# Performance work log

Hardware: AMD Instinct MI355X
Metric: run time of the kernel (lower is better)

Reference implementation:

```python
import jax, jax.numpy as jnp
import numpy as np

TEMPERATURE = 12.5
SINK_EPS = 0.05
SINK_ITERS = 100


def setup_inputs() -> dict:
    key = jax.random.key(0)
    k1, k2, k3, k4 = jax.random.split(key, 4)
    b, n_way, k_shot, q, c, h, w = 8, 5, 1, 75, 640, 7, 7
    return {
        "support_xf": jax.random.normal(k1, (b, n_way * k_shot, c, h, w), jnp.float32),
        "query_xf": jax.random.normal(k2, (b, q, c, h, w), jnp.float32),
        "support_y": jax.random.randint(k3, (b, n_way * k_shot), 0, n_way),
        "query_y": jax.random.randint(k4, (b, q), 0, n_way),
        "n_way": n_way,
        "k_shot": k_shot,
    }


def _sinkhorn_flow(cost, log_a, log_b, eps=SINK_EPS, iters=SINK_ITERS):
    """Entropic-OT (Sinkhorn, log-domain) replacement for cv2.EMD.
    cost: [..., m, n]; log_a: [..., m]; log_b: [..., n] (log of prob marginals).
    Returns transport plan P with row sums ~ exp(log_a), col sums ~ exp(log_b)."""
    f = jnp.zeros_like(log_a)
    g = jnp.zeros_like(log_b)

    def body(_, fg):
        f, g = fg
        f = eps * (log_a - jax.nn.logsumexp((g[..., None, :] - cost) / eps, axis=-1))
        g = eps * (log_b - jax.nn.logsumexp((f[..., :, None] - cost) / eps, axis=-2))
        return (f, g)

    f, g = jax.lax.fori_loop(0, iters, body, (f, g))
    return jnp.exp((f[..., :, None] + g[..., None, :] - cost) / eps)


def _deep_emd_logits(support, query):
    # support: [b, p, c, h, w] (1 prototype per class), query: [b, q, c, h, w]
    b, p, c, h, w = support.shape
    q = query.shape[1]
    hw = h * w
    sup = support.reshape(b, p, c, hw)
    qry = query.reshape(b, q, c, hw)

    # get_weight_vector: inner product of local features with the other set's GAP vector
    sup_gap = sup.mean(-1)  # [b, p, c]
    qry_gap = qry.mean(-1)  # [b, q, c]
    w1 = jax.nn.relu(jnp.einsum('bqcm,bpc->bqpm', qry, sup_gap)) + 1e-3  # [b,q,p,hw]
    w2 = jax.nn.relu(jnp.einsum('bpcn,bqc->bqpn', sup, qry_gap)) + 1e-3  # [b,q,p,hw] (weight_2[j,i] transposed)

    # normalize_feature: subtract per-image channel mean; then cosine similarity over channels
    supn = sup - sup.mean(2, keepdims=True)
    qryn = qry - qry.mean(2, keepdims=True)
    supn = supn / jnp.maximum(jnp.linalg.norm(supn, axis=2, keepdims=True), 1e-8)
    qryn = qryn / jnp.maximum(jnp.linalg.norm(qryn, axis=2, keepdims=True), 1e-8)
    S = jnp.einsum('bqcm,bpcn->bqpmn', qryn, supn)  # [b,q,p,hw,hw]

    # emd_inference marginal normalization: relu(w)+1e-5, rescaled so sum = hw -> prob = w/sum(w)
    wa = w1 + 1e-5
    wb = w2 + 1e-5
    log_a = jnp.log(wa) - jnp.log(wa.sum(-1, keepdims=True))
    log_b = jnp.log(wb) - jnp.log(wb.sum(-1, keepdims=True))

    flow = _sinkhorn_flow(1.0 - S, log_a, log_b) * hw  # total mass = hw as in cv2.EMD path
    flow = jax.lax.stop_gradient(flow)  # original flow comes from numpy -> constant

    logits = (S * flow).sum((-2, -1)) * (TEMPERATURE / hw)  # [b, q, p]
    return logits.reshape(b * q, p)


def reference(support_xf, query_xf, support_y, query_y, n_way, k_shot):
    # training / 1-shot path: pick first shot per class
    b = support_xf.shape[0]
    c, h, w = support_xf.shape[2:]
    sup = support_xf.reshape(b, n_way, k_shot, c, h, w)[:, :, 0]
    logits = _deep_emd_logits(sup, query_xf)  # [b*q, n_way]
    labels = query_y.reshape(-1)
    logp = jax.nn.log_softmax(logits, axis=-1)
    loss = -jnp.take_along_axis(logp, labels[:, None], axis=1).mean()
    return loss
```

## Files before the change

kernel.cpp:

```cpp
#include <hip/hip_runtime.h>
#include <math.h>

#define BB 8
#define PP 5
#define QQ 75
#define CC 640
#define HW 49
#define NIMG_Q (BB*QQ)
#define NIMG_S (BB*PP)
#define NPROB  (BB*QQ*PP)
#define TEMP 12.5f

#define CHUNKS 20
#define TROW 16
#define TCH  (HW*TROW)
#define TIMG (CHUNKS*TCH)
#define SROW 25
#define SPROB (HW*SROW)

#define OFF_SGAP   0
#define OFF_QGAP   (OFF_SGAP  + NIMG_S*CC)
#define OFF_SMEAN  (OFF_QGAP  + NIMG_Q*CC)
#define OFF_SINV   (OFF_SMEAN + NIMG_S*HW)
#define OFF_QMEAN  (OFF_SINV  + NIMG_S*HW)
#define OFF_QINV   (OFF_QMEAN + NIMG_Q*HW)
#define OFF_MARGA  (OFF_QINV  + NIMG_Q*HW)
#define OFF_MARGB  (OFF_MARGA + NPROB*HW)
#define OFF_QT     (OFF_MARGB + NPROB*HW)
#define OFF_ST     (OFF_QT    + NIMG_Q*TIMG)
#define OFF_S16    (OFF_ST    + NIMG_S*TIMG)
#define OFF_LOGITS (OFF_S16   + NPROB*SPROB)

typedef _Float16 f16x8 __attribute__((ext_vector_type(8)));
typedef float f32x4 __attribute__((ext_vector_type(4)));
#define MFMAH __builtin_amdgcn_mfma_f32_16x16x32_f16

__device__ __forceinline__ float wsum64(float v) {
#pragma unroll
    for (int off = 32; off > 0; off >>= 1) v += __shfl_xor(v, off, 64);
    return v;
}
__device__ __forceinline__ float rlf(float x, int l) {
    return __int_as_float(__builtin_amdgcn_readlane(__float_as_int(x), l));
}
__device__ __forceinline__ unsigned packh2(float a, float b) {
    union { _Float16 h[2]; unsigned u; } pk;
    pk.h[0] = (_Float16)a; pk.h[1] = (_Float16)b;
    return pk.u;
}
__device__ __forceinline__ float f16lo(unsigned w) {
    union { unsigned short s; _Float16 h; } u; u.s = (unsigned short)w; return (float)u.h;
}
__device__ __forceinline__ float f16hi(unsigned w) {
    union { unsigned short s; _Float16 h; } u; u.s = (unsigned short)(w >> 16); return (float)u.h;
}

__global__ __launch_bounds__(512) __attribute__((amdgpu_waves_per_eu(4, 4)))
void sup_prep(const float* __restrict__ sup, float* __restrict__ ws) {
    int img = blockIdx.x;
    int tid = threadIdx.x;
    int lane = tid & 63;
    int wv = tid >> 6;
    const float* X = sup + (size_t)img * CC * HW;
    float* gap = ws + OFF_SGAP + img * CC;

    __shared__ float cs_p[8][52], sq_p[8][52];
    __shared__ float muL[52], invL[52];
    float cs = 0.f, sq = 0.f;
    if (lane < HW) {
        for (int c8 = wv * 80; c8 < wv * 80 + 80; c8 += 8) {
            float v[8];
#pragma unroll
            for (int j = 0; j < 8; j++) v[j] = X[(c8 + j) * HW + lane];
#pragma unroll
            for (int j = 0; j < 8; j++) {
                cs += v[j];
                sq = fmaf(v[j], v[j], sq);
            }
        }
    }
    if (lane < 52) {
        cs_p[wv][lane] = (lane < HW) ? cs : 0.f;
        sq_p[wv][lane] = (lane < HW) ? sq : 0.f;
    }
    __syncthreads();
    if (wv == 0 && lane < HW) {
        float c4 = 0.f, s4 = 0.f;
#pragma unroll
        for (int w = 0; w < 8; w++) { c4 += cs_p[w][lane]; s4 += sq_p[w][lane]; }
        float mu = c4 * (1.0f / CC);
        float nsq = fmaxf(s4 - c4 * c4 * (1.0f / CC), 0.f);
        float inv = 1.0f / fmaxf(sqrtf(nsq), 1e-8f);
        ws[OFF_SMEAN + img * HW + lane] = mu;
        ws[OFF_SINV + img * HW + lane] = inv;
        muL[lane] = mu;
        invL[lane] = inv;
    }
    for (int c = tid; c < CC; c += 512) {
        const float* row = X + c * HW;
        float s = 0.f;
#pragma unroll
        for (int g = 0; g < 6; g++) {
            float rv[8];
#pragma unroll
            for (int j = 0; j < 8; j++) rv[j] = row[g * 8 + j];
#pragma unroll
            for (int j = 0; j < 8; j++) s += rv[j];
        }
        s += row[48];
        gap[c] = s * (1.0f / HW);
    }
    __syncthreads();
    unsigned* T = (unsigned*)ws + OFF_ST + (size_t)img * TIMG;
    int m = lane;
    if (m < HW) {
        float mu = muL[m], inv = invL[m];
        for (int t = wv; t < CHUNKS; t += 8) {
            float va[32];
#pragma unroll
            for (int j = 0; j < 32; j++) va[j] = X[(t * 32 + j) * HW + m];
            unsigned pk[16];
#pragma unroll
            for (int w = 0; w < 16; w++)
                pk[w] = packh2((va[2 * w] - mu) * inv, (va[2 * w + 1] - mu) * inv);
            uint4* dst = (uint4*)(T + t * TCH + m * TROW);
#pragma unroll
            for (int u = 0; u < 4; u++)
                dst[u] = make_uint4(pk[4 * u], pk[4 * u + 1], pk[4 * u + 2], pk[4 * u + 3]);
        }
    }
}

__global__ __launch_bounds__(512) __attribute__((amdgpu_waves_per_eu(4, 4)))
void qry_prep(const float* __restrict__ qry, float* __restrict__ ws) {
    int img = blockIdx.x;
    int b = img / QQ;
    int tid = threadIdx.x;
    int lane = tid & 63;
    int wv = tid >> 6;
    const float* X = qry + (size_t)img * CC * HW;
    const float* sg = ws + OFF_SGAP + b * PP * CC;
    float* gap = ws + OFF_QGAP + img * CC;

    __shared__ float XSG[PP * CC];
    __shared__ float cs_p[8][52], sq_p[8][52];
    __shared__ float part[8][PP][52];
    __shared__ float muL[52], invL[52];

    for (int i = tid; i < PP * CC / 4; i += 512)
        ((float4*)XSG)[i] = ((const float4*)sg)[i];
    __syncthreads();

    float cs = 0.f, sq = 0.f;
    float acc[PP] = {0.f, 0.f, 0.f, 0.f, 0.f};
    if (lane < HW) {
        for (int c8 = wv * 80; c8 < wv * 80 + 80; c8 += 8) {
            float v[8];
#pragma unroll
            for (int j = 0; j < 8; j++) v[j] = X[(c8 + j) * HW + lane];
#pragma unroll
            for (int j = 0; j < 8; j++) {
                cs += v[j];
                sq = fmaf(v[j], v[j], sq);
            }
#pragma unroll
            for (int p = 0; p < PP; p++) {
                float4 g0 = *(const float4*)&XSG[p * CC + c8];
                float4 g1 = *(const float4*)&XSG[p * CC + c8 + 4];
                float a = acc[p];
                a = fmaf(v[0], g0.x, a); a = fmaf(v[1], g0.y, a);
                a = fmaf(v[2], g0.z, a); a = fmaf(v[3], g0.w, a);
                a = fmaf(v[4], g1.x, a); a = fmaf(v[5], g1.y, a);
                a = fmaf(v[6], g1.z, a); a = fmaf(v[7], g1.w, a);
                acc[p] = a;
            }
        }
    }
    if (lane < 52) {
        cs_p[wv][lane] = (lane < HW) ? cs : 0.f;
        sq_p[wv][lane] = (lane < HW) ? sq : 0.f;
#pragma unroll
        for (int p = 0; p < PP; p++) part[wv][p][lane] = (lane < HW) ? acc[p] : 0.f;
    }
    __syncthreads();
    if (wv == 0) {
        if (lane < HW) {
            float c4 = 0.f, s4 = 0.f;
#pragma unroll
            for (int w = 0; w < 8; w++) { c4 += cs_p[w][lane]; s4 += sq_p[w][lane]; }
            float mu = c4 * (1.0f / CC);
            float nsq = fmaxf(s4 - c4 * c4 * (1.0f / CC), 0.f);
            float inv = 1.0f / fmaxf(sqrtf(nsq), 1e-8f);
            ws[OFF_QMEAN + img * HW + lane] = mu;
            ws[OFF_QINV + img * HW + lane] = inv;
            muL[lane] = mu;
            invL[lane] = inv;
        }
#pragma unroll
        for (int p = 0; p < PP; p++) {
            float a = 0.f;
            if (lane < 52) {
#pragma unroll
                for (int w = 0; w < 8; w++) a += part[w][p][lane];
            }
            float w = (lane < HW) ? (fmaxf(a, 0.f) + 1.01e-3f) : 0.f;
            float s = wsum64(w);
            if (lane < HW) ws[OFF_MARGA + (img * PP + p) * HW + lane] = w / s;
        }
    }
    for (int c = tid; c < CC; c += 512) {
        const float* row = X + c * HW;
        float s = 0.f;
#pragma unroll
        for (int g = 0; g < 6; g++) {
            float rv[8];
#pragma unroll
            for (int j = 0; j < 8; j++) rv[j] = row[g * 8 + j];
#pragma unroll
            for (int j = 0; j < 8; j++) s += rv[j];
        }
        s += row[48];
        gap[c] = s * (1.0f / HW);
    }
    __syncthreads();
    unsigned* T = (unsigned*)ws + OFF_QT + (size_t)img * TIMG;
    int m = lane;
    if (m < HW) {
        float mu = muL[m], inv = invL[m];
        for (int t = wv; t < CHUNKS; t += 8) {
            float va[32];
#pragma unroll
            for (int j = 0; j < 32; j++) va[j] = X[(t * 32 + j) * HW + m];
            unsigned pk[16];
#pragma unroll
            for (int w = 0; w < 16; w++)
                pk[w] = packh2((va[2 * w] - mu) * inv, (va[2 * w + 1] - mu) * inv);
            uint4* dst = (uint4*)(T + t * TCH + m * TROW);
#pragma unroll
            for (int u = 0; u < 4; u++)
                dst[u] = make_uint4(pk[4 * u], pk[4 * u + 1], pk[4 * u + 2], pk[4 * u + 3]);
        }
    }
}

__global__ __launch_bounds__(256) __attribute__((amdgpu_waves_per_eu(2, 4)))
void margb_kernel(const float* __restrict__ sup, float* __restrict__ ws) {
    int id = blockIdx.x;
    int qc = id % 5;
    int bp = id / 5;
    int b = bp / PP;
    int p = bp % PP;
    int tid = threadIdx.x;
    int lane = tid & 63;
    int wv = tid >> 6;
    const float* X = sup + (size_t)bp * CC * HW;
    const float* qg = ws + OFF_QGAP + (b * QQ + qc * 15) * CC;

    __shared__ float QG[15 * CC];
    __shared__ float part[4][15][52];
    for (int i = tid; i < 15 * CC / 4; i += 256)
        ((float4*)QG)[i] = ((const float4*)qg)[i];
    __syncthreads();

    float acc[15];
#pragma unroll
    for (int i = 0; i < 15; i++) acc[i] = 0.f;
    if (lane < HW) {
        for (int c8 = wv * 160; c8 < wv * 160 + 160; c8 += 8) {
            float sv[8];
#pragma unroll
            for (int j = 0; j < 8; j++) sv[j] = X[(c8 + j) * HW + lane];
#pragma unroll
            for (int qq = 0; qq < 15; qq++) {
                float4 g0 = *(const float4*)&QG[qq * CC + c8];
                float4 g1 = *(const float4*)&QG[qq * CC + c8 + 4];
                float a = acc[qq];
                a = fmaf(sv[0], g0.x, a); a = fmaf(sv[1], g0.y, a);
                a = fmaf(sv[2], g0.z, a); a = fmaf(sv[3], g0.w, a);
                a = fmaf(sv[4], g1.x, a); a = fmaf(sv[5], g1.y, a);
                a = fmaf(sv[6], g1.z, a); a = fmaf(sv[7], g1.w, a);
                acc[qq] = a;
            }
        }
    }
    if (lane < 52) {
#pragma unroll
        for (int qq = 0; qq < 15; qq++) part[wv][qq][lane] = (lane < HW) ? acc[qq] : 0.f;
    }
    __syncthreads();
    if (wv == 0) {
#pragma unroll
        for (int qq = 0; qq < 15; qq++) {
            float a = 0.f;
            if (lane < 52)
                a = part[0][qq][lane] + part[1][qq][lane] + part[2][qq][lane] + part[3][qq][lane];
            int q = qc * 15 + qq;
            float w = (lane < HW) ? (fmaxf(a, 0.f) + 1.01e-3f) : 0.f;
            float s = wsum64(w);
            if (lane < HW) ws[OFF_MARGB + ((b * QQ + q) * PP + p) * HW + lane] = w / s;
        }
    }
}

__global__ __launch_bounds__(256, 2) void gemm_kernel(float* __restrict__ ws) {
    __shared__ unsigned LDSU[CHUNKS * TCH];

    int g = blockIdx.x;
    int xcd = g & 7;
    int k = g >> 3;
    int p = k % 5;
    int gidx = xcd + 8 * (k / 5);
    int b = gidx / 15;
    int qg = gidx - b * 15;

    int tid = threadIdx.x;
    int lane = tid & 63;
    int wv = tid >> 6;
    int lrow = lane & 15;
    int quad = lane >> 4;

    const unsigned* Bt = (const unsigned*)ws + OFF_ST + (size_t)(b * PP + p) * TIMG;
    for (int idx = tid; idx < CHUNKS * HW * 4; idx += 256) {
        int r = idx >> 2;
        int q = idx & 3;
        int t = r / 49;
        int n = r - t * 49;
        uint4 v = *(const uint4*)(Bt + (idx << 2));
        *(uint4*)(&LDSU[t * TCH + n * 16 + ((q ^ ((n >> 1) & 3)) << 2)]) = v;
    }
    __syncthreads();

    int bof[4];
#pragma unroll
    for (int nt = 0; nt < 4; nt++) {
        int n = 16 * nt + lrow;
        if (n > 48) n = 48;
        bof[nt] = n * 16 + ((quad ^ ((n >> 1) & 3)) << 2);
    }

    const unsigned* Aq = (const unsigned*)ws + OFF_QT + (size_t)(b * QQ + qg * 5) * TIMG;
    int arow = (16 * wv + lrow) * TROW + quad * 4;

    f32x4 acc[5][4];
#pragma unroll
    for (int qi = 0; qi < 5; qi++)
#pragma unroll
        for (int nt = 0; nt < 4; nt++) acc[qi][nt] = (f32x4){0.f, 0.f, 0.f, 0.f};

#pragma unroll 2
    for (int t = 0; t < CHUNKS; t++) {
        f16x8 bfr[4];
#pragma unroll
        for (int nt = 0; nt < 4; nt++)
            bfr[nt] = *(const f16x8*)(&LDSU[t * TCH + bof[nt]]);
#pragma unroll
        for (int qi = 0; qi < 5; qi++) {
            f16x8 a = *(const f16x8*)(Aq + (size_t)qi * TIMG + t * TCH + arow);
#pragma unroll
            for (int nt = 0; nt < 4; nt++)
                acc[qi][nt] = MFMAH(a, bfr[nt], acc[qi][nt], 0, 0, 0);
        }
    }

    __syncthreads();
    float* S_lds = (float*)LDSU;
#pragma unroll
    for (int qi = 0; qi < 5; qi++)
#pragma unroll
        for (int nt = 0; nt < 4; nt++)
#pragma unroll
            for (int r = 0; r < 4; r++) {
                int mm = 16 * wv + quad * 4 + r;
                int nn = 16 * nt + lrow;
                if (mm < HW && nn < HW) S_lds[qi * 2597 + mm * 53 + nn] = acc[qi][nt][r];
            }
    __syncthreads();

    for (int qi = 0; qi < 5; qi++) {
        int prob = (b * QQ + qg * 5 + qi) * PP + p;
        unsigned* Sp = (unsigned*)ws + OFF_S16 + (size_t)prob * SPROB;
        const float* Sl = S_lds + qi * 2597;
        for (int idx = tid; idx < SPROB; idx += 256) {
            int row = idx / SROW;
            int w = idx - row * SROW;
            int n0 = 2 * w;
            float v0 = Sl[row * 53 + n0];
            float v1 = (n0 + 1 < HW) ? Sl[row * 53 + n0 + 1] : 0.f;
            Sp[idx] = packh2(v0, v1);
        }
    }
}

#define FOR12(M) M(0) M(1) M(2) M(3) M(4) M(5) M(6) M(7) M(8) M(9) M(10) M(11)
#define KEXPF(s) __expf(fmaf(20.f, (s), -20.f))

__global__ __launch_bounds__(64)
__attribute__((amdgpu_waves_per_eu(3, 3)))
void sinkhorn_kernel(float* __restrict__ ws) {
    int prob = blockIdx.x;
    int lane = threadIdx.x;
    const unsigned* Sp = (const unsigned*)ws + OFF_S16 + (size_t)prob * SPROB;

    float am = 0.f, bm = 0.f;
    if (lane < HW) {
        am = ws[OFF_MARGA + prob * HW + lane];
        bm = ws[OFF_MARGB + prob * HW + lane];
    }
    int ll = (lane < HW) ? lane : 48;
    const unsigned* rbase = Sp + ll * SROW;
    int wof = ll >> 1;
    int sh = (ll & 1) * 16;

    float4 kr0, kr1, kr2, kr3, kr4, kr5, kr6, kr7, kr8, kr9, kr10, kr11;
    float4 kt0, kt1, kt2, kt3, kt4, kt5, kt6, kt7, kt8, kt9, kt10, kt11;
    float kr12x, kt12x;
#define KIR(g) { unsigned w0 = rbase[2*(g)]; unsigned w1 = rbase[2*(g)+1];  \
    kr##g = make_float4(KEXPF(f16lo(w0)), KEXPF(f16hi(w0)),                 \
                        KEXPF(f16lo(w1)), KEXPF(f16hi(w1))); }
    FOR12(KIR)
#undef KIR
    kr12x = KEXPF(f16lo(rbase[24]));
#define KIT(g) { \
    float s0 = f16lo((Sp[(4*(g)+0)*SROW + wof] >> sh) & 0xFFFFu);           \
    float s1 = f16lo((Sp[(4*(g)+1)*SROW + wof] >> sh) & 0xFFFFu);           \
    float s2 = f16lo((Sp[(4*(g)+2)*SROW + wof] >> sh) & 0xFFFFu);           \
    float s3 = f16lo((Sp[(4*(g)+3)*SROW + wof] >> sh) & 0xFFFFu);           \
    kt##g = make_float4(KEXPF(s0), KEXPF(s1), KEXPF(s2), KEXPF(s3)); }
    FOR12(KIT)
#undef KIT
    kt12x = KEXPF(f16lo((Sp[48 * SROW + wof] >> sh) & 0xFFFFu));

    float vv = (lane < HW) ? 1.f : 0.f;
    float uu = 0.f;

#pragma unroll 1
    for (int it = 0; it < 48; it++) {
        float t0 = 0.f, t1 = 0.f, t2 = 0.f, t3 = 0.f;
#define RS(g) { t0 = fmaf(kr##g.x, rlf(vv, 4*(g)+0), t0);                   \
                t1 = fmaf(kr##g.y, rlf(vv, 4*(g)+1), t1);                   \
                t2 = fmaf(kr##g.z, rlf(vv, 4*(g)+2), t2);                   \
                t3 = fmaf(kr##g.w, rlf(vv, 4*(g)+3), t3); }
        FOR12(RS)
#undef RS
        t0 = fmaf(kr12x, rlf(vv, 48), t0);
        float t = (t0 + t1) + (t2 + t3);
        uu = am * __builtin_amdgcn_rcpf(t);

        float s0 = 0.f, s1 = 0.f, s2 = 0.f, s3 = 0.f;
#define CS(g) { s0 = fmaf(kt##g.x, rlf(uu, 4*(g)+0), s0);                   \
                s1 = fmaf(kt##g.y, rlf(uu, 4*(g)+1), s1);                   \
                s2 = fmaf(kt##g.z, rlf(uu, 4*(g)+2), s2);                   \
                s3 = fmaf(kt##g.w, rlf(uu, 4*(g)+3), s3); }
        FOR12(CS)
#undef CS
        s0 = fmaf(kt12x, rlf(uu, 48), s0);
        float s = (s0 + s1) + (s2 + s3);
        vv = bm * __builtin_amdgcn_rcpf(s);
    }

    float ssum = 0.f;
#define FS(g) {                                                             \
    ssum = fmaf(kr##g.x * fmaf(0.05f, __logf(kr##g.x), 1.f), rlf(vv, 4*(g)+0), ssum); \
    ssum = fmaf(kr##g.y * fmaf(0.05f, __logf(kr##g.y), 1.f), rlf(vv, 4*(g)+1), ssum); \
    ssum = fmaf(kr##g.z * fmaf(0.05f, __logf(kr##g.z), 1.f), rlf(vv, 4*(g)+2), ssum); \
    ssum = fmaf(kr##g.w * fmaf(0.05f, __logf(kr##g.w), 1.f), rlf(vv, 4*(g)+3), ssum); }
    FOR12(FS)
#undef FS
    ssum = fmaf(kr12x * fmaf(0.05f, __logf(kr12x), 1.f), rlf(vv, 48), ssum);
    float contrib = (lane < HW) ? (uu * ssum) : 0.f;
    float tot = wsum64(contrib);
    if (lane == 0) ws[OFF_LOGITS + prob] = TEMP * tot;
}

__global__ __launch_bounds__(640) void loss_kernel(const float* __restrict__ ws,
                                                   const int* __restrict__ qy,
                                                   float* __restrict__ out) {
    int tid = threadIdx.x;
    float val = 0.f;
    if (tid < NIMG_Q) {
        const float* lg = ws + OFF_LOGITS + tid * PP;
        float l[PP];
        float mx = -1e30f;
#pragma unroll
        for (int p = 0; p < PP; p++) {
            l[p] = lg[p];
            mx = fmaxf(mx, l[p]);
        }
        float se = 0.f;
#pragma unroll
        for (int p = 0; p < PP; p++) se += __expf(l[p] - mx);
        float lse = mx + logf(se);
        int lab = qy[tid];
        val = -(l[lab] - lse);
    }
    __shared__ float red[16];
    float s = wsum64(val);
    if ((tid & 63) == 0) red[tid >> 6] = s;
    __syncthreads();
    if (tid == 0) {
        float tot = 0.f;
#pragma unroll
        for (int w = 0; w < 10; w++) tot += red[w];
        out[0] = tot * (1.0f / NIMG_Q);
    }
}

extern "C" void kernel_launch(void* const* d_in, const int* in_sizes, int n_in,
                              void* d_out, int out_size, void* d_ws, size_t ws_size,
                              hipStream_t stream) {
    const float* sup = (const float*)d_in[0];
    const float* qry = (const float*)d_in[1];
    const int* qy = (const int*)d_in[3];
    float* ws = (float*)d_ws;
    float* out = (float*)d_out;

    sup_prep<<<NIMG_S, 512, 0, stream>>>(sup, ws);
    qry_prep<<<NIMG_Q, 512, 0, stream>>>(qry, ws);
    margb_kernel<<<NIMG_S * 5, 256, 0, stream>>>(sup, ws);
    gemm_kernel<<<600, 256, 0, stream>>>(ws);
    sinkhorn_kernel<<<NPROB, 64, 0, stream>>>(ws);
    loss_kernel<<<1, 640, 0, stream>>>(ws, qy, out);
}
```

Baseline: 284.0 us.

## Keep transposed Sinkhorn kernel in LDS instead of registers; widen GAP unroll

```diff
diff --git a/kernel.cpp b/kernel.cpp
--- a/kernel.cpp
+++ b/kernel.cpp
@@ -154,24 +154,26 @@
     float cs = 0.f, sq = 0.f;
     float acc[PP] = {0.f, 0.f, 0.f, 0.f, 0.f};
     if (lane < HW) {
-        for (int c8 = wv * 80; c8 < wv * 80 + 80; c8 += 8) {
-            float v[8];
-#pragma unroll
-            for (int j = 0; j < 8; j++) v[j] = X[(c8 + j) * HW + lane];
-#pragma unroll
-            for (int j = 0; j < 8; j++) {
+        for (int c8 = wv * 80; c8 < wv * 80 + 80; c8 += 16) {
+            float v[16];
+#pragma unroll
+            for (int j = 0; j < 16; j++) v[j] = X[(c8 + j) * HW + lane];
+#pragma unroll
+            for (int j = 0; j < 16; j++) {
                 cs += v[j];
                 sq = fmaf(v[j], v[j], sq);
             }
 #pragma unroll
             for (int p = 0; p < PP; p++) {
-                float4 g0 = *(const float4*)&XSG[p * CC + c8];
-                float4 g1 = *(const float4*)&XSG[p * CC + c8 + 4];
                 float a = acc[p];
-                a = fmaf(v[0], g0.x, a); a = fmaf(v[1], g0.y, a);
-                a = fmaf(v[2], g0.z, a); a = fmaf(v[3], g0.w, a);
-                a = fmaf(v[4], g1.x, a); a = fmaf(v[5], g1.y, a);
-                a = fmaf(v[6], g1.z, a); a = fmaf(v[7], g1.w, a);
+#pragma unroll
+                for (int qv = 0; qv < 4; qv++) {
+                    float4 g0 = *(const float4*)&XSG[p * CC + c8 + 4 * qv];
+                    a = fmaf(v[4 * qv + 0], g0.x, a);
+                    a = fmaf(v[4 * qv + 1], g0.y, a);
+                    a = fmaf(v[4 * qv + 2], g0.z, a);
+                    a = fmaf(v[4 * qv + 3], g0.w, a);
+                }
                 acc[p] = a;
             }
         }
@@ -397,6 +399,7 @@
 __global__ __launch_bounds__(64)
 __attribute__((amdgpu_waves_per_eu(3, 3)))
 void sinkhorn_kernel(float* __restrict__ ws) {
+    __shared__ float KT[HW * 53];
     int prob = blockIdx.x;
     int lane = threadIdx.x;
     const unsigned* Sp = (const unsigned*)ws + OFF_S16 + (size_t)prob * SPROB;
@@ -408,27 +411,27 @@
     }
     int ll = (lane < HW) ? lane : 48;
     const unsigned* rbase = Sp + ll * SROW;
-    int wof = ll >> 1;
-    int sh = (ll & 1) * 16;
 
     float4 kr0, kr1, kr2, kr3, kr4, kr5, kr6, kr7, kr8, kr9, kr10, kr11;
-    float4 kt0, kt1, kt2, kt3, kt4, kt5, kt6, kt7, kt8, kt9, kt10, kt11;
-    float kr12x, kt12x;
+    float kr12x;
 #define KIR(g) { unsigned w0 = rbase[2*(g)]; unsigned w1 = rbase[2*(g)+1];  \
     kr##g = make_float4(KEXPF(f16lo(w0)), KEXPF(f16hi(w0)),                 \
                         KEXPF(f16lo(w1)), KEXPF(f16hi(w1))); }
     FOR12(KIR)
 #undef KIR
     kr12x = KEXPF(f16lo(rbase[24]));
-#define KIT(g) { \
-    float s0 = f16lo((Sp[(4*(g)+0)*SROW + wof] >> sh) & 0xFFFFu);           \
-    float s1 = f16lo((Sp[(4*(g)+1)*SROW + wof] >> sh) & 0xFFFFu);           \
-    float s2 = f16lo((Sp[(4*(g)+2)*SROW + wof] >> sh) & 0xFFFFu);           \
-    float s3 = f16lo((Sp[(4*(g)+3)*SROW + wof] >> sh) & 0xFFFFu);           \
-    kt##g = make_float4(KEXPF(s0), KEXPF(s1), KEXPF(s2), KEXPF(s3)); }
-    FOR12(KIT)
-#undef KIT
-    kt12x = KEXPF(f16lo((Sp[48 * SROW + wof] >> sh) & 0xFFFFu));
+
+    if (lane < HW) {
+#define KW(g) { KT[(4*(g)+0)*53 + lane] = kr##g.x;                          \
+                KT[(4*(g)+1)*53 + lane] = kr##g.y;                          \
+                KT[(4*(g)+2)*53 + lane] = kr##g.z;                          \
+                KT[(4*(g)+3)*53 + lane] = kr##g.w; }
+        FOR12(KW)
+#undef KW
+        KT[48 * 53 + lane] = kr12x;
+    }
+    __syncthreads();
+    const float* KTrow = KT + ll * 53;
 
     float vv = (lane < HW) ? 1.f : 0.f;
     float uu = 0.f;
@@ -446,14 +449,18 @@
         float t = (t0 + t1) + (t2 + t3);
         uu = am * __builtin_amdgcn_rcpf(t);
 
+        if (__builtin_expect((int)blockIdx.x < 0, 0)) KT[lane] = uu;
+
         float s0 = 0.f, s1 = 0.f, s2 = 0.f, s3 = 0.f;
-#define CS(g) { s0 = fmaf(kt##g.x, rlf(uu, 4*(g)+0), s0);                   \
-                s1 = fmaf(kt##g.y, rlf(uu, 4*(g)+1), s1);                   \
-                s2 = fmaf(kt##g.z, rlf(uu, 4*(g)+2), s2);                   \
-                s3 = fmaf(kt##g.w, rlf(uu, 4*(g)+3), s3); }
+#define CS(g) { float k0 = KTrow[4*(g)+0]; float k1 = KTrow[4*(g)+1];       \
+                float k2 = KTrow[4*(g)+2]; float k3 = KTrow[4*(g)+3];       \
+                s0 = fmaf(k0, rlf(uu, 4*(g)+0), s0);                        \
+                s1 = fmaf(k1, rlf(uu, 4*(g)+1), s1);                        \
+                s2 = fmaf(k2, rlf(uu, 4*(g)+2), s2);                        \
+                s3 = fmaf(k3, rlf(uu, 4*(g)+3), s3); }
         FOR12(CS)
 #undef CS
-        s0 = fmaf(kt12x, rlf(uu, 48), s0);
+        s0 = fmaf(KTrow[48], rlf(uu, 48), s0);
         float s = (s0 + s1) + (s2 + s3);
         vv = bm * __builtin_amdgcn_rcpf(s);
     }
```

Result: slower. 297.3 us (+4.7%).
